# Performance work log

Measured on AMD Instinct MI355X. Metric: run time of the kernel, lower is better.

The kernel has to match this reference:

```python
import jax, jax.numpy as jnp
import numpy as np

EPS = 1e-10
TEMP = 1.0


def setup_inputs() -> dict:
    key = jax.random.key(0)
    ks = jax.random.split(key, 8)
    num_nodes, embed_dim, hidden_dim, num_edges = 50000, 128, 64, 600000
    node_embed = jax.random.normal(ks[0], (num_nodes, embed_dim), dtype=jnp.float32)
    edge_index = jax.random.randint(ks[1], (2, num_edges), 0, num_nodes, dtype=jnp.int64)
    u1 = jax.random.uniform(ks[2], (num_edges,), dtype=jnp.float32)
    u2 = jax.random.uniform(ks[3], (num_edges,), dtype=jnp.float32)
    # Linear weights (kaiming-ish scale)
    W1 = jax.random.normal(ks[4], (2 * embed_dim, hidden_dim), dtype=jnp.float32) * (1.0 / np.sqrt(2 * embed_dim))
    b1 = jnp.zeros((hidden_dim,), dtype=jnp.float32)
    W2 = jax.random.normal(ks[5], (hidden_dim, 1), dtype=jnp.float32) * (1.0 / np.sqrt(hidden_dim))
    b2 = jnp.zeros((1,), dtype=jnp.float32)
    return {"node_embed": node_embed, "edge_index": edge_index, "u1": u1, "u2": u2,
            "W1": W1, "b1": b1, "W2": W2, "b2": b2}


def reference(node_embed, edge_index, u1, u2, W1, b1, W2, b2):
    row, col = edge_index[0], edge_index[1]
    # gather + concat: [num_edges, 2*embed_dim]
    edge_feat = jnp.concatenate([node_embed[row], node_embed[col]], axis=1)
    # small MLP (dropout is identity in eval)
    h = jax.nn.relu(edge_feat @ W1 + b1)
    edge_logits = (h @ W2 + b2).squeeze(-1)  # [num_edges]
    # Gumbel-sigmoid (soft)
    g1 = -jnp.log(-jnp.log(jnp.clip(u1, EPS, 1.0 - EPS)))
    g2 = -jnp.log(-jnp.log(jnp.clip(u2, EPS, 1.0 - EPS)))
    edge_probs = jax.nn.sigmoid((edge_logits + g1 - g2) / TEMP)
    return edge_probs
```

## Files before the change

kernel.cpp:

```cpp
#include <hip/hip_runtime.h>
#include <stdint.h>

typedef float  floatx4 __attribute__((ext_vector_type(4)));
typedef short  short8  __attribute__((ext_vector_type(8)));
typedef float  f4v     __attribute__((ext_vector_type(4)));
typedef unsigned int uint32;

#define GS_EPS 1e-10f

__device__ __forceinline__ unsigned short f2bf(float x) {
  uint32 u = __float_as_uint(x);
  u += 0x7FFFu + ((u >> 16) & 1u);
  return (unsigned short)(u >> 16);
}
__device__ __forceinline__ float bf2f(short v) {
  return __uint_as_float(((uint32)(unsigned short)v) << 16);
}

__global__ void conv_w1cat_kernel(const float* __restrict__ W1,
                                  unsigned short* __restrict__ w1g) {
  int i = blockIdx.x * 256 + threadIdx.x;
  int chunk = i >> 7;
  int n = i & 127;
  const float* src = (n < 64) ? (W1 + n) : (W1 + 128 * 64 + (n - 64));
  uint32 d[4];
#pragma unroll
  for (int j = 0; j < 4; ++j) {
    int k0 = chunk * 8 + 2 * j;
    unsigned short lo = f2bf(src[(size_t)k0 * 64]);
    unsigned short hi = f2bf(src[(size_t)(k0 + 1) * 64]);
    d[j] = (uint32)lo | ((uint32)hi << 16);
  }
#pragma unroll
  for (int j = 0; j < 4; ++j) *(uint32*)&w1g[(size_t)i * 8 + 2 * j] = d[j];
}

__global__ __launch_bounds__(512, 4) void pcompute_kernel(
    const float* __restrict__ E, const unsigned short* __restrict__ w1g,
    const float* __restrict__ b1, unsigned short* __restrict__ P,
    int num_nodes) {
  __shared__ __align__(16) unsigned short w1blk[16 * 128 * 8];

  const int tid = threadIdx.x;
  const int wave = tid >> 6;
  const int lane = tid & 63;
  const int q = lane >> 4;
  const int l16 = lane & 15;

#pragma unroll
  for (int it = 0; it < 4; ++it) {
    int idx = it * 512 + tid;
    short8 v = *(const short8*)(w1g + (size_t)idx * 8);
    *(short8*)&w1blk[(size_t)idx * 8] = v;
  }

  const int rowbase = blockIdx.x * 128 + wave * 16;
  int row = rowbase + l16;
  const bool ok = row < num_nodes;
  if (!ok) row = num_nodes - 1;

  short8 bfr[4];
#pragma unroll
  for (int kk = 0; kk < 4; ++kk) {
    const float* p = E + (size_t)row * 128 + kk * 32 + q * 8;
    f4v v0 = *(const f4v*)p;
    f4v v1 = *(const f4v*)(p + 4);
    short8 t;
    t[0] = (short)f2bf(v0[0]); t[1] = (short)f2bf(v0[1]);
    t[2] = (short)f2bf(v0[2]); t[3] = (short)f2bf(v0[3]);
    t[4] = (short)f2bf(v1[0]); t[5] = (short)f2bf(v1[1]);
    t[6] = (short)f2bf(v1[2]); t[7] = (short)f2bf(v1[3]);
    bfr[kk] = t;
  }
  __syncthreads();

  floatx4 acc[8];
#pragma unroll
  for (int t = 0; t < 8; ++t) {
    floatx4 z = {0.f, 0.f, 0.f, 0.f};
    acc[t] = z;
  }
#pragma unroll
  for (int kk = 0; kk < 4; ++kk) {
#pragma unroll
    for (int t = 0; t < 8; ++t) {
      short8 af = *(const short8*)&w1blk[(size_t)((kk * 4 + q) * 128 + t * 16 + l16) * 8];
      acc[t] = __builtin_amdgcn_mfma_f32_16x16x32_bf16(af, bfr[kk], acc[t], 0, 0, 0);
    }
  }

#pragma unroll
  for (int t = 0; t < 8; ++t) {
    floatx4 a = acc[t];
    if (t < 4) {
      f4v bv = *(const f4v*)(b1 + t * 16 + q * 4);
      a[0] += bv[0]; a[1] += bv[1]; a[2] += bv[2]; a[3] += bv[3];
    }
    uint32 lo = (uint32)f2bf(a[0]) | ((uint32)f2bf(a[1]) << 16);
    uint32 hi = (uint32)f2bf(a[2]) | ((uint32)f2bf(a[3]) << 16);
    if (ok) {
      uint32* dst = (uint32*)(P + (size_t)(rowbase + l16) * 128 + t * 16 + q * 4);
      dst[0] = lo;
      dst[1] = hi;
    }
  }
}

__global__ __launch_bounds__(256, 8) void edge_kernel(
    const unsigned short* __restrict__ P,
    const int* __restrict__ ei,
    const float* __restrict__ u1, const float* __restrict__ u2,
    const float* __restrict__ W2, const float* __restrict__ b2,
    float* __restrict__ out, int num_edges) {
  const int tid = threadIdx.x;
  const int wave = tid >> 6;
  const int lane = tid & 63;
  const int g = lane >> 3;
  const int h = lane & 7;
  const int wbase = blockIdx.x * 128 + wave * 32;

  f4v w0 = *(const f4v*)(W2 + h * 8);
  f4v w1v = *(const f4v*)(W2 + h * 8 + 4);
  const float bias2 = b2[0];

  int el = wbase + (lane & 31);
  if (el > num_edges - 1) el = num_edges - 1;
  unsigned long long oddmask = __ballot(ei[2 * el + 1] != 0);
  const bool idx64 = (oddmask == 0ULL);
  int eR, eC;
  if (idx64) {
    eR = ei[2 * el];
    eC = ei[2 * (num_edges + el)];
  } else {
    eR = ei[el];
    eC = ei[num_edges + el];
  }

  short8 ar[4], ac[4];
#pragma unroll
  for (int s = 0; s < 4; ++s) {
    int nr = __shfl(eR, s * 8 + g, 64);
    int nc = __shfl(eC, s * 8 + g, 64);
    ar[s] = *(const short8*)(P + (size_t)nr * 128 + h * 8);
    ac[s] = *(const short8*)(P + (size_t)nc * 128 + 64 + h * 8);
  }

#pragma unroll
  for (int s = 0; s < 4; ++s) {
    float acc = 0.f;
#pragma unroll
    for (int j = 0; j < 8; ++j) {
      float hv = fmaxf(bf2f(ar[s][j]) + bf2f(ac[s][j]), 0.f);
      float ww = (j < 4) ? w0[j] : w1v[j - 4];
      acc = fmaf(hv, ww, acc);
    }
    acc += __shfl_xor(acc, 1, 64);
    acc += __shfl_xor(acc, 2, 64);
    acc += __shfl_xor(acc, 4, 64);
    if (h == 0) {
      int e = wbase + s * 8 + g;
      if (e < num_edges) {
        float a1 = fminf(fmaxf(u1[e], GS_EPS), 1.0f);
        float a2 = fminf(fmaxf(u2[e], GS_EPS), 1.0f);
        float g1 = -__logf(-__logf(a1));
        float g2 = -__logf(-__logf(a2));
        float x = acc + bias2 + g1 - g2;
        out[e] = 1.f / (1.f + __expf(-x));
      }
    }
  }
}

extern "C" void kernel_launch(void* const* d_in, const int* in_sizes, int n_in,
                              void* d_out, int out_size, void* d_ws, size_t ws_size,
                              hipStream_t stream) {
  const float* node_embed = (const float*)d_in[0];
  const int* ei = (const int*)d_in[1];
  const float* u1 = (const float*)d_in[2];
  const float* u2 = (const float*)d_in[3];
  const float* W1 = (const float*)d_in[4];
  const float* b1 = (const float*)d_in[5];
  const float* W2 = (const float*)d_in[6];
  const float* b2 = (const float*)d_in[7];
  float* out = (float*)d_out;

  const int num_edges = in_sizes[2];
  const int num_nodes = in_sizes[0] / 128;

  unsigned short* P = (unsigned short*)d_ws;
  const size_t p_bytes = (size_t)num_nodes * 128 * sizeof(unsigned short);
  unsigned short* w1g = (unsigned short*)((char*)d_ws + ((p_bytes + 255) & ~(size_t)255));

  conv_w1cat_kernel<<<8, 256, 0, stream>>>(W1, w1g);
  const int pblocks = (num_nodes + 127) / 128;
  pcompute_kernel<<<pblocks, 512, 0, stream>>>(node_embed, w1g, b1, P, num_nodes);
  const int eblocks = (num_edges + 127) / 128;
  edge_kernel<<<eblocks, 256, 0, stream>>>(P, ei, u1, u2, W2, b2, out, num_edges);
}
```

Baseline: 116.1 us.

## Quantize per-node projections to int8 with global absmax scales for edge gathers

The pcompute kernel now tracks the global absolute maximum of the row-half and column-half projections with atomicMax. A new quant kernel converts the bf16 projection table to int8 using those two scales. The edge kernel then gathers 8-byte int8 chunks instead of 16-byte bf16 chunks and dequantizes in registers, halving the random-gather traffic. This costs an extra kernel launch and a full pass over P, plus a precision loss from per-tensor int8 quantization.

```diff
diff --git a/kernel.cpp b/kernel.cpp
--- a/kernel.cpp
+++ b/kernel.cpp
@@ -16,9 +16,15 @@
 __device__ __forceinline__ float bf2f(short v) {
   return __uint_as_float(((uint32)(unsigned short)v) << 16);
 }
+__device__ __forceinline__ float i8tof(uint32 w, int j) {
+  int b = (int)(w << (24 - 8 * j)) >> 24;
+  return (float)b;
+}
 
 __global__ void conv_w1cat_kernel(const float* __restrict__ W1,
-                                  unsigned short* __restrict__ w1g) {
+                                  unsigned short* __restrict__ w1g,
+                                  uint32* __restrict__ gmax) {
+  if (blockIdx.x == 0 && threadIdx.x < 2) gmax[threadIdx.x] = 0u;
   int i = blockIdx.x * 256 + threadIdx.x;
   int chunk = i >> 7;
   int n = i & 127;
@@ -38,7 +44,7 @@
 __global__ __launch_bounds__(512, 4) void pcompute_kernel(
     const float* __restrict__ E, const unsigned short* __restrict__ w1g,
     const float* __restrict__ b1, unsigned short* __restrict__ P,
-    int num_nodes) {
+    uint32* __restrict__ gmax, int num_nodes) {
   __shared__ __align__(16) unsigned short w1blk[16 * 128 * 8];
 
   const int tid = threadIdx.x;
@@ -89,6 +95,7 @@
     }
   }
 
+  float mtop = 0.f, mbot = 0.f;
 #pragma unroll
   for (int t = 0; t < 8; ++t) {
     floatx4 a = acc[t];
@@ -96,6 +103,8 @@
       f4v bv = *(const f4v*)(b1 + t * 16 + q * 4);
       a[0] += bv[0]; a[1] += bv[1]; a[2] += bv[2]; a[3] += bv[3];
     }
+    float m = fmaxf(fmaxf(fabsf(a[0]), fabsf(a[1])), fmaxf(fabsf(a[2]), fabsf(a[3])));
+    if (t < 4) mtop = fmaxf(mtop, m); else mbot = fmaxf(mbot, m);
     uint32 lo = (uint32)f2bf(a[0]) | ((uint32)f2bf(a[1]) << 16);
     uint32 hi = (uint32)f2bf(a[2]) | ((uint32)f2bf(a[3]) << 16);
     if (ok) {
@@ -104,10 +113,49 @@
       dst[1] = hi;
     }
   }
+#pragma unroll
+  for (int s = 1; s < 64; s <<= 1) {
+    mtop = fmaxf(mtop, __shfl_xor(mtop, s, 64));
+    mbot = fmaxf(mbot, __shfl_xor(mbot, s, 64));
+  }
+  if (lane == 0) {
+    atomicMax(&gmax[0], __float_as_uint(mtop));
+    atomicMax(&gmax[1], __float_as_uint(mbot));
+  }
+}
+
+__global__ __launch_bounds__(256) void quant_kernel(
+    const unsigned short* __restrict__ P, const uint32* __restrict__ gmax,
+    uint8_t* __restrict__ P8, int total16) {
+  int i = blockIdx.x * 256 + threadIdx.x;
+  if (i >= total16) return;
+  const float at = __uint_as_float(gmax[0]);
+  const float ab = __uint_as_float(gmax[1]);
+  const float invt = 127.f / fmaxf(at, 1e-20f);
+  const float invb = 127.f / fmaxf(ab, 1e-20f);
+  const float inv = ((i & 7) < 4) ? invt : invb;
+  const size_t off = (size_t)i * 16;
+  short8 v0 = *(const short8*)(P + off);
+  short8 v1 = *(const short8*)(P + off + 8);
+  uint32 outw[4];
+#pragma unroll
+  for (int w = 0; w < 4; ++w) {
+    uint32 r = 0;
+#pragma unroll
+    for (int j = 0; j < 4; ++j) {
+      short s = (w < 2) ? v0[w * 4 + j] : v1[(w - 2) * 4 + j];
+      float x = bf2f(s) * inv;
+      x = fminf(fmaxf(x, -127.f), 127.f);
+      int vq = (int)__builtin_rintf(x);
+      r |= ((uint32)(vq & 255)) << (8 * j);
+    }
+    outw[w] = r;
+  }
+  *(uint4*)(P8 + off) = *(uint4*)outw;
 }
 
 __global__ __launch_bounds__(256, 8) void edge_kernel(
-    const unsigned short* __restrict__ P,
+    const uint8_t* __restrict__ P8, const uint32* __restrict__ gmax,
     const int* __restrict__ ei,
     const float* __restrict__ u1, const float* __restrict__ u2,
     const float* __restrict__ W2, const float* __restrict__ b2,
@@ -119,6 +167,8 @@
   const int h = lane & 7;
   const int wbase = blockIdx.x * 128 + wave * 32;
 
+  const float st = __uint_as_float(gmax[0]) * (1.f / 127.f);
+  const float sb = __uint_as_float(gmax[1]) * (1.f / 127.f);
   f4v w0 = *(const f4v*)(W2 + h * 8);
   f4v w1v = *(const f4v*)(W2 + h * 8 + 4);
   const float bias2 = b2[0];
@@ -136,27 +186,31 @@
     eC = ei[num_edges + el];
   }
 
-  short8 ar[4], ac[4];
+  uint2 ar[4], ac[4];
 #pragma unroll
   for (int s = 0; s < 4; ++s) {
     int nr = __shfl(eR, s * 8 + g, 64);
     int nc = __shfl(eC, s * 8 + g, 64);
-    ar[s] = *(const short8*)(P + (size_t)nr * 128 + h * 8);
-    ac[s] = *(const short8*)(P + (size_t)nc * 128 + 64 + h * 8);
+    ar[s] = *(const uint2*)(P8 + (size_t)nr * 128 + h * 8);
+    ac[s] = *(const uint2*)(P8 + (size_t)nc * 128 + 64 + h * 8);
   }
 
 #pragma unroll
   for (int s = 0; s < 4; ++s) {
-    float acc = 0.f;
-#pragma unroll
-    for (int j = 0; j < 8; ++j) {
-      float hv = fmaxf(bf2f(ar[s][j]) + bf2f(ac[s][j]), 0.f);
-      float ww = (j < 4) ? w0[j] : w1v[j - 4];
-      acc = fmaf(hv, ww, acc);
-    }
-    acc += __shfl_xor(acc, 1, 64);
-    acc += __shfl_xor(acc, 2, 64);
-    acc += __shfl_xor(acc, 4, 64);
+    float accv = 0.f;
+#pragma unroll
+    for (int j = 0; j < 4; ++j) {
+      float hv = fmaxf(i8tof(ar[s].x, j) * st + i8tof(ac[s].x, j) * sb, 0.f);
+      accv = fmaf(hv, w0[j], accv);
+    }
+#pragma unroll
+    for (int j = 0; j < 4; ++j) {
+      float hv = fmaxf(i8tof(ar[s].y, j) * st + i8tof(ac[s].y, j) * sb, 0.f);
+      accv = fmaf(hv, w1v[j], accv);
+    }
+    accv += __shfl_xor(accv, 1, 64);
+    accv += __shfl_xor(accv, 2, 64);
+    accv += __shfl_xor(accv, 4, 64);
     if (h == 0) {
       int e = wbase + s * 8 + g;
       if (e < num_edges) {
@@ -164,7 +218,7 @@
         float a2 = fminf(fmaxf(u2[e], GS_EPS), 1.0f);
         float g1 = -__logf(-__logf(a1));
         float g2 = -__logf(-__logf(a2));
-        float x = acc + bias2 + g1 - g2;
+        float x = accv + bias2 + g1 - g2;
         out[e] = 1.f / (1.f + __expf(-x));
       }
     }
@@ -187,13 +241,17 @@
   const int num_edges = in_sizes[2];
   const int num_nodes = in_sizes[0] / 128;
 
-  unsigned short* P = (unsigned short*)d_ws;
-  const size_t p_bytes = (size_t)num_nodes * 128 * sizeof(unsigned short);
-  unsigned short* w1g = (unsigned short*)((char*)d_ws + ((p_bytes + 255) & ~(size_t)255));
-
-  conv_w1cat_kernel<<<8, 256, 0, stream>>>(W1, w1g);
+  char* w = (char*)d_ws;
+  unsigned short* P = (unsigned short*)w;   w += ((size_t)num_nodes * 128 * 2 + 255) & ~(size_t)255;
+  uint8_t* P8 = (uint8_t*)w;                w += ((size_t)num_nodes * 128 + 255) & ~(size_t)255;
+  uint32* gmax = (uint32*)w;                w += 256;
+  unsigned short* w1g = (unsigned short*)w;
+
+  conv_w1cat_kernel<<<8, 256, 0, stream>>>(W1, w1g, gmax);
   const int pblocks = (num_nodes + 127) / 128;
-  pcompute_kernel<<<pblocks, 512, 0, stream>>>(node_embed, w1g, b1, P, num_nodes);
+  pcompute_kernel<<<pblocks, 512, 0, stream>>>(node_embed, w1g, b1, P, gmax, num_nodes);
+  const int total16 = num_nodes * 8;
+  quant_kernel<<<(total16 + 255) / 256, 256, 0, stream>>>(P, gmax, P8, total16);
   const int eblocks = (num_edges + 127) / 128;
-  edge_kernel<<<eblocks, 256, 0, stream>>>(P, ei, u1, u2, W2, b2, out, num_edges);
-}
+  edge_kernel<<<eblocks, 256, 0, stream>>>(P8, gmax, ei, u1, u2, W2, b2, out, num_edges);
+}
```

Result: slower. 183.8 us (+58.4%).
